# Kernel optimization log

Hardware: AMD Instinct MI355X
Metric: run time of the kernel (lower is better)

Reference implementation:

```python
import jax, jax.numpy as jnp
import numpy as np

T, I, H = 4096, 2048, 2048


def setup_inputs() -> dict:
    key = jax.random.key(0)
    ks = jax.random.split(key, 7)
    s = 0.075
    return {
        "x": jax.random.normal(ks[0], (1, T, I), dtype=jnp.float32),
        "W_ih": jax.random.normal(ks[1], (4 * H, I), dtype=jnp.float32) * s,
        "W_hh": jax.random.normal(ks[2], (4 * H, H), dtype=jnp.float32) * s,
        "b_ih": jax.random.normal(ks[3], (4 * H,), dtype=jnp.float32) * s,
        "b_hh": jax.random.normal(ks[4], (4 * H,), dtype=jnp.float32) * s,
        "Wo": jax.random.normal(ks[5], (I, H), dtype=jnp.float32) * s,
        "bo": jax.random.normal(ks[6], (I,), dtype=jnp.float32) * s,
    }


def reference(x, W_ih, W_hh, b_ih, b_hh, Wo, bo):
    xs = x[0]  # [T, I]  (batch dim of 1 squeezed, as in original)
    # Precompute input projections for all timesteps in one big GEMM: [T, 4H]
    gx = xs @ W_ih.T + (b_ih + b_hh)

    def step(carry, gxt):
        h, c = carry  # [H], [H]
        g = gxt + W_hh @ h  # [4H]; PyTorch gate order: i, f, g, o
        i_g, f_g, g_g, o_g = jnp.split(g, 4)
        c_new = jax.nn.sigmoid(f_g) * c + jax.nn.sigmoid(i_g) * jnp.tanh(g_g)
        h_new = jax.nn.sigmoid(o_g) * jnp.tanh(c_new)
        return (h_new, c_new), h_new

    h0 = jnp.zeros((H,), dtype=x.dtype)
    c0 = jnp.zeros((H,), dtype=x.dtype)
    _, hs = jax.lax.scan(step, (h0, c0), gx)  # hs: [T, H]

    out = jax.nn.sigmoid(hs @ Wo.T + bo)  # [T, I]
    return out[None]  # [1, T, I]
```

## Files before the change

kernel.cpp:

```cpp
#include <hip/hip_runtime.h>

#define T_STEPS 4096
#define IDIM 2048
#define HDIM 2048
#define G4DIM 8192

typedef __attribute__((ext_vector_type(8))) short short8;
typedef __attribute__((ext_vector_type(4))) float f32x4;
typedef __attribute__((ext_vector_type(2))) float f32x2;

__device__ __forceinline__ unsigned short f2bf(float f) {
  unsigned int u = __float_as_uint(f);
  u += 0x7fffu + ((u >> 16) & 1u);
  return (unsigned short)(u >> 16);
}
__device__ __forceinline__ float bf2f(unsigned short h) {
  return __uint_as_float(((unsigned int)h) << 16);
}

template <int ACT_SIGMOID, int OUT_BF16>
__global__ __launch_bounds__(256) void gemm_bt(
    const float* __restrict__ A, const float* __restrict__ B,
    const float* __restrict__ bias, void* __restrict__ Cout,
    int M, int N, int K)
{
  __shared__ short Ah[64][40];
  __shared__ short Al[64][40];
  __shared__ short Bh[64][40];
  __shared__ short Bl[64][40];
  const int tid  = threadIdx.x;
  const int wave = tid >> 6, lane = tid & 63;
  const int bn = blockIdx.x * 64, bm = blockIdx.y * 64;
  const int srow = tid >> 2, sc8 = (tid & 3) * 8;
  const int wm = (wave >> 1) * 32, wn = (wave & 1) * 32;
  const int lq = lane >> 4, lr = lane & 15;
  f32x4 acc[2][2] = {};

  for (int k0 = 0; k0 < K; k0 += 32) {
    __syncthreads();
    {
      const float* src = A + (size_t)(bm + srow) * K + k0 + sc8;
      float4 v0 = *(const float4*)(src);
      float4 v1 = *(const float4*)(src + 4);
      float vv[8] = {v0.x, v0.y, v0.z, v0.w, v1.x, v1.y, v1.z, v1.w};
      short8 vh, vl;
      #pragma unroll
      for (int i = 0; i < 8; ++i) {
        unsigned short hb = f2bf(vv[i]);
        vh[i] = (short)hb;
        vl[i] = (short)f2bf(vv[i] - bf2f(hb));
      }
      *(short8*)&Ah[srow][sc8] = vh;
      *(short8*)&Al[srow][sc8] = vl;
    }
    {
      const float* src = B + (size_t)(bn + srow) * K + k0 + sc8;
      float4 v0 = *(const float4*)(src);
      float4 v1 = *(const float4*)(src + 4);
      float vv[8] = {v0.x, v0.y, v0.z, v0.w, v1.x, v1.y, v1.z, v1.w};
      short8 vh, vl;
      #pragma unroll
      for (int i = 0; i < 8; ++i) {
        unsigned short hb = f2bf(vv[i]);
        vh[i] = (short)hb;
        vl[i] = (short)f2bf(vv[i] - bf2f(hb));
      }
      *(short8*)&Bh[srow][sc8] = vh;
      *(short8*)&Bl[srow][sc8] = vl;
    }
    __syncthreads();

    short8 ah0 = *(const short8*)&Ah[wm +      lr][lq * 8];
    short8 al0 = *(const short8*)&Al[wm +      lr][lq * 8];
    short8 ah1 = *(const short8*)&Ah[wm + 16 + lr][lq * 8];
    short8 al1 = *(const short8*)&Al[wm + 16 + lr][lq * 8];
    short8 bh0 = *(const short8*)&Bh[wn +      lr][lq * 8];
    short8 bl0 = *(const short8*)&Bl[wn +      lr][lq * 8];
    short8 bh1 = *(const short8*)&Bh[wn + 16 + lr][lq * 8];
    short8 bl1 = *(const short8*)&Bl[wn + 16 + lr][lq * 8];

    acc[0][0] = __builtin_amdgcn_mfma_f32_16x16x32_bf16(ah0, bh0, acc[0][0], 0, 0, 0);
    acc[0][0] = __builtin_amdgcn_mfma_f32_16x16x32_bf16(ah0, bl0, acc[0][0], 0, 0, 0);
    acc[0][0] = __builtin_amdgcn_mfma_f32_16x16x32_bf16(al0, bh0, acc[0][0], 0, 0, 0);

    acc[0][1] = __builtin_amdgcn_mfma_f32_16x16x32_bf16(ah0, bh1, acc[0][1], 0, 0, 0);
    acc[0][1] = __builtin_amdgcn_mfma_f32_16x16x32_bf16(ah0, bl1, acc[0][1], 0, 0, 0);
    acc[0][1] = __builtin_amdgcn_mfma_f32_16x16x32_bf16(al0, bh1, acc[0][1], 0, 0, 0);

    acc[1][0] = __builtin_amdgcn_mfma_f32_16x16x32_bf16(ah1, bh0, acc[1][0], 0, 0, 0);
    acc[1][0] = __builtin_amdgcn_mfma_f32_16x16x32_bf16(ah1, bl0, acc[1][0], 0, 0, 0);
    acc[1][0] = __builtin_amdgcn_mfma_f32_16x16x32_bf16(al1, bh0, acc[1][0], 0, 0, 0);

    acc[1][1] = __builtin_amdgcn_mfma_f32_16x16x32_bf16(ah1, bh1, acc[1][1], 0, 0, 0);
    acc[1][1] = __builtin_amdgcn_mfma_f32_16x16x32_bf16(ah1, bl1, acc[1][1], 0, 0, 0);
    acc[1][1] = __builtin_amdgcn_mfma_f32_16x16x32_bf16(al1, bh1, acc[1][1], 0, 0, 0);
  }

  #pragma unroll
  for (int mi = 0; mi < 2; ++mi) {
    #pragma unroll
    for (int ni = 0; ni < 2; ++ni) {
      #pragma unroll
      for (int rr = 0; rr < 4; ++rr) {
        int row = bm + wm + mi * 16 + lq * 4 + rr;
        int col = bn + wn + ni * 16 + lr;
        float v = acc[mi][ni][rr];
        if (bias) v += bias[col];
        if (ACT_SIGMOID) v = 1.f / (1.f + __expf(-v));
        if (OUT_BF16)
          ((unsigned short*)Cout)[(size_t)row * N + col] = f2bf(v);
        else
          ((float*)Cout)[(size_t)row * N + col] = v;
      }
    }
  }
}

__global__ __launch_bounds__(1024, 4) void lstm_scan(
    const float* __restrict__ Whh,
    const float* __restrict__ b_ih, const float* __restrict__ b_hh,
    const unsigned short* __restrict__ gx,
    float* __restrict__ hs)
{
  const int b   = blockIdx.x;
  const int tid = threadIdx.x;
  const int u   = tid & 7;
  const int kc  = tid >> 3;
  const int wv  = tid >> 6;

  f32x2 w2[4][8];
  #pragma unroll
  for (int g = 0; g < 4; ++g) {
    const float* wp = Whh + (size_t)(g * HDIM + b * 8 + u) * HDIM + kc * 16;
    #pragma unroll
    for (int i = 0; i < 4; ++i) {
      float4 v = *(const float4*)(wp + 4 * i);
      w2[g][2 * i]     = f32x2{v.x, v.y};
      w2[g][2 * i + 1] = f32x2{v.z, v.w};
    }
  }
  float bias_r = 0.f;
  if (tid < 32) {
    int br = (tid >> 3) * HDIM + b * 8 + (tid & 7);
    bias_r = b_ih[br] + b_hh[br];
  }
  float cval = 0.f;

  __shared__ float h_lds[128 * 20];
  __shared__ float partials[2][16][33];
  unsigned int* hs_u = (unsigned int*)hs;

  for (int t = 0; t < T_STEPS; ++t) {
    float gxv = 0.f;
    if (tid < 32)
      gxv = bf2f(gx[(size_t)t * G4DIM + (tid >> 3) * HDIM + b * 8 + (tid & 7)]);

    f32x2 h2w;
    if (t > 0) {
      const unsigned int* p = hs_u + (size_t)(t - 1) * HDIM + tid * 2;
      unsigned int u0, u1;
      for (;;) {
        u0 = __hip_atomic_load(p + 0, __ATOMIC_RELAXED, __HIP_MEMORY_SCOPE_AGENT);
        u1 = __hip_atomic_load(p + 1, __ATOMIC_RELAXED, __HIP_MEMORY_SCOPE_AGENT);
        if (u0 != 0xAAAAAAAAu && u1 != 0xAAAAAAAAu) break;
        __builtin_amdgcn_s_sleep(1);
      }
      h2w = f32x2{__uint_as_float(u0), __uint_as_float(u1)};
    } else {
      h2w = f32x2{0.f, 0.f};
    }

    *(f32x2*)&h_lds[kc * 20 + u * 2] = h2w;

    f32x2 acc0{0.f, 0.f}, acc1{0.f, 0.f}, acc2{0.f, 0.f}, acc3{0.f, 0.f};
    #pragma unroll
    for (int i = 0; i < 4; ++i) {
      float4 hv = *(const float4*)&h_lds[kc * 20 + i * 4];
      f32x2 ha{hv.x, hv.y}, hb{hv.z, hv.w};
      acc0 += w2[0][2 * i] * ha;  acc0 += w2[0][2 * i + 1] * hb;
      acc1 += w2[1][2 * i] * ha;  acc1 += w2[1][2 * i + 1] * hb;
      acc2 += w2[2][2 * i] * ha;  acc2 += w2[2][2 * i + 1] * hb;
      acc3 += w2[3][2 * i] * ha;  acc3 += w2[3][2 * i + 1] * hb;
    }
    float s0 = acc0[0] + acc0[1];
    float s1 = acc1[0] + acc1[1];
    float s2 = acc2[0] + acc2[1];
    float s3 = acc3[0] + acc3[1];
    #pragma unroll
    for (int m = 8; m <= 32; m <<= 1) {
      s0 += __shfl_xor(s0, m, 64);
      s1 += __shfl_xor(s1, m, 64);
      s2 += __shfl_xor(s2, m, 64);
      s3 += __shfl_xor(s3, m, 64);
    }
    if ((tid & 56) == 0) {
      partials[t & 1][wv][0 * 8 + u] = s0;
      partials[t & 1][wv][1 * 8 + u] = s1;
      partials[t & 1][wv][2 * 8 + u] = s2;
      partials[t & 1][wv][3 * 8 + u] = s3;
    }
    __syncthreads();

    if (tid < 64) {
      float gval = 0.f;
      if (tid < 32) {
        float s = gxv + bias_r;
        #pragma unroll
        for (int q = 0; q < 16; ++q) s += partials[t & 1][q][tid];
        gval = s;
      }
      float g_i = __shfl(gval, tid);
      float g_f = __shfl(gval, tid + 8);
      float g_g = __shfl(gval, tid + 16);
      float g_o = __shfl(gval, tid + 24);
      if (tid < 8) {
        float is = 1.f / (1.f + __expf(-g_i));
        float fs = 1.f / (1.f + __expf(-g_f));
        float os = 1.f / (1.f + __expf(-g_o));
        float e2 = __expf(-2.f * fabsf(g_g));
        float tg = (1.f - e2) / (1.f + e2);
        tg = (g_g < 0.f) ? -tg : tg;
        float cn = fs * cval + is * tg;
        cval = cn;
        float ec = __expf(-2.f * fabsf(cn));
        float tc = (1.f - ec) / (1.f + ec);
        tc = (cn < 0.f) ? -tc : tc;
        float hn = os * tc;
        __hip_atomic_store(hs_u + (size_t)t * HDIM + b * 8 + tid,
                           __float_as_uint(hn),
                           __ATOMIC_RELAXED, __HIP_MEMORY_SCOPE_AGENT);
      }
    }
  }
}

extern "C" void kernel_launch(void* const* d_in, const int* in_sizes, int n_in,
                              void* d_out, int out_size, void* d_ws, size_t ws_size,
                              hipStream_t stream) {
  (void)in_sizes; (void)n_in; (void)out_size; (void)ws_size;
  const float* x    = (const float*)d_in[0];
  const float* W_ih = (const float*)d_in[1];
  const float* W_hh = (const float*)d_in[2];
  const float* b_ih = (const float*)d_in[3];
  const float* b_hh = (const float*)d_in[4];
  const float* Wo   = (const float*)d_in[5];
  const float* bo   = (const float*)d_in[6];
  float* out = (float*)d_out;

  char* ws = (char*)d_ws;
  unsigned short* gx = (unsigned short*)ws;
  float* hs = (float*)(ws + (size_t)T_STEPS * G4DIM * 2);

  hipMemsetAsync(hs, 0xAA, (size_t)T_STEPS * HDIM * sizeof(float), stream);

  gemm_bt<0, 1><<<dim3(G4DIM / 64, T_STEPS / 64), 256, 0, stream>>>(
      x, W_ih, nullptr, gx, T_STEPS, G4DIM, IDIM);

  lstm_scan<<<256, 1024, 0, stream>>>(W_hh, b_ih, b_hh, gx, hs);

  gemm_bt<1, 0><<<dim3(IDIM / 64, T_STEPS / 64), 256, 0, stream>>>(
      hs, Wo, bo, out, T_STEPS, IDIM, HDIM);
}
```

Before: 12.65 ms.

## Delegate cross-block hidden-state polling to one wave, publishing via LDS double buffer

Before, all 1024 threads in every block polled global memory for the previous hidden state and then staged it into LDS. Now a single wave (wave 15) polls, checking the tail of each 128-element segment first and then any words still holding the poison value. It writes h for the next step into a double-buffered LDS array and signals the other waves with a workgroup-scope release flag, which they spin on in LDS. This is meant to cut global/L2 polling traffic and contention across the whole grid, at the cost of serialising the h fetch through one wave and adding a flag handshake on the critical path.

```diff
diff --git a/kernel.cpp b/kernel.cpp
--- a/kernel.cpp
+++ b/kernel.cpp
@@ -4,6 +4,7 @@
 #define IDIM 2048
 #define HDIM 2048
 #define G4DIM 8192
+#define POISON 0xAAAAAAAAu
 
 typedef __attribute__((ext_vector_type(8))) short short8;
 typedef __attribute__((ext_vector_type(4))) float f32x4;
@@ -122,11 +123,12 @@
     const unsigned short* __restrict__ gx,
     float* __restrict__ hs)
 {
-  const int b   = blockIdx.x;
-  const int tid = threadIdx.x;
-  const int u   = tid & 7;
-  const int kc  = tid >> 3;
-  const int wv  = tid >> 6;
+  const int b    = blockIdx.x;
+  const int tid  = threadIdx.x;
+  const int u    = tid & 7;
+  const int kc   = tid >> 3;
+  const int wv   = tid >> 6;
+  const int lane = tid & 63;
 
   f32x2 w2[4][8];
   #pragma unroll
@@ -146,8 +148,14 @@
   }
   float cval = 0.f;
 
-  __shared__ float h_lds[128 * 20];
+  __shared__ float hbuf[2][128 * 20];
   __shared__ float partials[2][16][33];
+  __shared__ int sh_flag;
+
+  for (int i = tid; i < 128 * 20; i += 1024) hbuf[0][i] = 0.f;
+  if (tid == 0) sh_flag = 0;
+  __syncthreads();
+
   unsigned int* hs_u = (unsigned int*)hs;
 
   for (int t = 0; t < T_STEPS; ++t) {
@@ -155,32 +163,20 @@
     if (tid < 32)
       gxv = bf2f(gx[(size_t)t * G4DIM + (tid >> 3) * HDIM + b * 8 + (tid & 7)]);
 
-    f32x2 h2w;
-    if (t > 0) {
-      const unsigned int* p = hs_u + (size_t)(t - 1) * HDIM + tid * 2;
-      unsigned int u0, u1;
-      for (;;) {
-        u0 = __hip_atomic_load(p + 0, __ATOMIC_RELAXED, __HIP_MEMORY_SCOPE_AGENT);
-        u1 = __hip_atomic_load(p + 1, __ATOMIC_RELAXED, __HIP_MEMORY_SCOPE_AGENT);
-        if (u0 != 0xAAAAAAAAu && u1 != 0xAAAAAAAAu) break;
-        __builtin_amdgcn_s_sleep(1);
-      }
-      h2w = f32x2{__uint_as_float(u0), __uint_as_float(u1)};
-    } else {
-      h2w = f32x2{0.f, 0.f};
-    }
-
-    *(f32x2*)&h_lds[kc * 20 + u * 2] = h2w;
-
+    while (__hip_atomic_load(&sh_flag, __ATOMIC_ACQUIRE,
+                             __HIP_MEMORY_SCOPE_WORKGROUP) < t)
+      __builtin_amdgcn_s_sleep(1);
+
+    const float* hb = hbuf[t & 1];
     f32x2 acc0{0.f, 0.f}, acc1{0.f, 0.f}, acc2{0.f, 0.f}, acc3{0.f, 0.f};
     #pragma unroll
     for (int i = 0; i < 4; ++i) {
-      float4 hv = *(const float4*)&h_lds[kc * 20 + i * 4];
-      f32x2 ha{hv.x, hv.y}, hb{hv.z, hv.w};
-      acc0 += w2[0][2 * i] * ha;  acc0 += w2[0][2 * i + 1] * hb;
-      acc1 += w2[1][2 * i] * ha;  acc1 += w2[1][2 * i + 1] * hb;
-      acc2 += w2[2][2 * i] * ha;  acc2 += w2[2][2 * i + 1] * hb;
-      acc3 += w2[3][2 * i] * ha;  acc3 += w2[3][2 * i + 1] * hb;
+      float4 hv = *(const float4*)&hb[kc * 20 + i * 4];
+      f32x2 ha{hv.x, hv.y}, hc{hv.z, hv.w};
+      acc0 += w2[0][2 * i] * ha;  acc0 += w2[0][2 * i + 1] * hc;
+      acc1 += w2[1][2 * i] * ha;  acc1 += w2[1][2 * i + 1] * hc;
+      acc2 += w2[2][2 * i] * ha;  acc2 += w2[2][2 * i + 1] * hc;
+      acc3 += w2[3][2 * i] * ha;  acc3 += w2[3][2 * i + 1] * hc;
     }
     float s0 = acc0[0] + acc0[1];
     float s1 = acc1[0] + acc1[1];
@@ -201,7 +197,7 @@
     }
     __syncthreads();
 
-    if (tid < 64) {
+    if (wv == 0) {
       float gval = 0.f;
       if (tid < 32) {
         float s = gxv + bias_r;
@@ -230,6 +226,49 @@
                            __float_as_uint(hn),
                            __ATOMIC_RELAXED, __HIP_MEMORY_SCOPE_AGENT);
       }
+    } else if (wv == 15 && t + 1 < T_STEPS) {
+      const unsigned int* src = hs_u + (size_t)t * HDIM;
+      if (lane < 16) {
+        const unsigned int* sp = src + lane * 128 + 127;
+        while (__hip_atomic_load(sp, __ATOMIC_RELAXED,
+                                 __HIP_MEMORY_SCOPE_AGENT) == POISON)
+          __builtin_amdgcn_s_sleep(2);
+      }
+      uint4 gv[8];
+      const uint4* s4 = (const uint4*)(src + lane * 32);
+      #pragma unroll
+      for (int g = 0; g < 8; ++g) gv[g] = s4[g];
+      for (;;) {
+        unsigned pend = 0;
+        #pragma unroll
+        for (int g = 0; g < 8; ++g)
+          if (gv[g].x == POISON || gv[g].y == POISON ||
+              gv[g].z == POISON || gv[g].w == POISON) pend |= 1u << g;
+        if (__ballot(pend != 0) == 0ull) break;
+        #pragma unroll
+        for (int g = 0; g < 8; ++g) {
+          if (pend & (1u << g)) {
+            const unsigned int* q = src + lane * 32 + g * 4;
+            gv[g].x = __hip_atomic_load(q + 0, __ATOMIC_RELAXED, __HIP_MEMORY_SCOPE_AGENT);
+            gv[g].y = __hip_atomic_load(q + 1, __ATOMIC_RELAXED, __HIP_MEMORY_SCOPE_AGENT);
+            gv[g].z = __hip_atomic_load(q + 2, __ATOMIC_RELAXED, __HIP_MEMORY_SCOPE_AGENT);
+            gv[g].w = __hip_atomic_load(q + 3, __ATOMIC_RELAXED, __HIP_MEMORY_SCOPE_AGENT);
+          }
+        }
+        __builtin_amdgcn_s_sleep(1);
+      }
+      float* dst = hbuf[(t + 1) & 1];
+      #pragma unroll
+      for (int g = 0; g < 8; ++g) {
+        float4 w4;
+        w4.x = __uint_as_float(gv[g].x); w4.y = __uint_as_float(gv[g].y);
+        w4.z = __uint_as_float(gv[g].z); w4.w = __uint_as_float(gv[g].w);
+        *(float4*)&dst[(2 * lane + (g >> 2)) * 20 + (g & 3) * 4] = w4;
+      }
+      __threadfence_block();
+      if (lane == 0)
+        __hip_atomic_store(&sh_flag, t + 1, __ATOMIC_RELEASE,
+                           __HIP_MEMORY_SCOPE_WORKGROUP);
     }
   }
 }
```

Result: slower. 16.70 ms (+32.0%).
